# Optimization experiments

Measured on AMD Instinct MI355X. Metric: run time of the kernel, lower is better.

Reference implementation:

```python
import jax, jax.numpy as jnp
import numpy as np

V = 50000      # word vocab
CV = 63        # char vocab (60 chars + 3 tags)
HW = 512       # word hidden size
HC = 256       # char hidden size
NLW = 2        # word lstm layers
NLC = 2        # char lstm layers
L = 12         # chars in the word


def _lstm_layers(x, H, C, Wih, Whh, bih, bhh):
    """One time-step of a multi-layer LSTM (PyTorch gate order i,f,g,o).
    x: [1, D], H/C: [nl, 1, D]. Returns (top_h, newH, newC)."""
    nl = Wih.shape[0]
    newH, newC = [], []
    inp = x
    for l in range(nl):
        gates = inp @ Wih[l].T + H[l] @ Whh[l].T + bih[l] + bhh[l]  # [1, 4D]
        i, f, g, o = jnp.split(gates, 4, axis=-1)
        i = jax.nn.sigmoid(i)
        f = jax.nn.sigmoid(f)
        g = jnp.tanh(g)
        o = jax.nn.sigmoid(o)
        c = f * C[l] + i * g
        h = o * jnp.tanh(c)
        newH.append(h)
        newC.append(c)
        inp = h
    return inp, jnp.stack(newH), jnp.stack(newC)


def setup_inputs() -> dict:
    key = jax.random.key(0)
    ks = jax.random.split(key, 20)
    sW = 1.0 / np.sqrt(HW)
    sC = 1.0 / np.sqrt(HC)
    return {
        "x_word": jax.random.randint(ks[0], (1,), 0, V),
        "x_char": jax.random.randint(ks[1], (L,), 0, CV),
        "h_word_h": jax.random.normal(ks[2], (NLW, 1, HW), jnp.float32),
        "h_word_c": jax.random.normal(ks[3], (NLW, 1, HW), jnp.float32),
        "h_char_h": jax.random.normal(ks[4], (NLC, 1, HC), jnp.float32),
        "h_char_c": jax.random.normal(ks[5], (NLC, 1, HC), jnp.float32),
        "word_emb": jax.random.normal(ks[6], (V, HW), jnp.float32),
        "word_Wih": jax.random.normal(ks[7], (NLW, 4 * HW, HW), jnp.float32) * sW,
        "word_Whh": jax.random.normal(ks[8], (NLW, 4 * HW, HW), jnp.float32) * sW,
        "word_bih": jax.random.normal(ks[9], (NLW, 4 * HW), jnp.float32) * sW,
        "word_bhh": jax.random.normal(ks[10], (NLW, 4 * HW), jnp.float32) * sW,
        "dec_W": jax.random.normal(ks[11], (V, HW), jnp.float32) * sW,
        "dec_b": jax.random.normal(ks[12], (V,), jnp.float32) * sW,
        "char_emb": jax.random.normal(ks[13], (CV, HC), jnp.float32),
        "char_Wih": jax.random.normal(ks[14], (NLC, 4 * HC, HC), jnp.float32) * sC,
        "char_Whh": jax.random.normal(ks[15], (NLC, 4 * HC, HC), jnp.float32) * sC,
        "char_bih": jax.random.normal(ks[16], (NLC, 4 * HC), jnp.float32) * sC,
        "char_bhh": jax.random.normal(ks[17], (NLC, 4 * HC), jnp.float32) * sC,
        "char_to_embedding": jax.random.normal(ks[18], (HW, HC), jnp.float32),
        "g_w": jax.random.normal(ks[19], (HW,), jnp.float32) * sW,
        "g_b": jax.random.normal(jax.random.fold_in(key, 99), (1,), jnp.float32),
    }


def reference(x_word, x_char, h_word_h, h_word_c, h_char_h, h_char_c,
              word_emb, word_Wih, word_Whh, word_bih, word_bhh,
              dec_W, dec_b,
              char_emb, char_Wih, char_Whh, char_bih, char_bhh,
              char_to_embedding, g_w, g_b):
    # character-level recurrence over the word's characters
    def char_step(carry, cidx):
        H, C = carry
        xc = char_emb[cidx][None, :]  # [1, HC]
        _, H, C = _lstm_layers(xc, H, C, char_Wih, char_Whh, char_bih, char_bhh)
        return (H, C), None

    (h_char_h, h_char_c), _ = jax.lax.scan(char_step, (h_char_h, h_char_c), x_char)

    # note: original uses h_char[1] (the CELL state) of the last layer
    x_c = char_to_embedding @ h_char_c[-1].T          # [HW, 1]
    x_w = word_emb[x_word[0]][None, :]                # [1, HW]
    g = jax.nn.relu(jnp.dot(g_w, x_w[0]) + g_b[0])    # scalar gate
    x = (1.0 - g) * x_w + g * x_c.T                   # [1, HW]

    y, h_word_h, h_word_c = _lstm_layers(x, h_word_h, h_word_c,
                                         word_Wih, word_Whh, word_bih, word_bhh)
    y = y @ dec_W.T + dec_b                           # [1, V]
    return y, h_word_h, h_word_c, h_char_h, h_char_c
```

## Files before the change

### kernel.cpp

```cpp
#include <hip/hip_runtime.h>
#include <stdint.h>


static __device__ __forceinline__ float dot4(float4 w, const float* p){
    return w.x*p[0] + w.y*p[1] + w.z*p[2] + w.w*p[3];
}
static __device__ __forceinline__ float sigf(float x){ return 1.0f / (1.0f + __expf(-x)); }
static __device__ __forceinline__ float tanhf_(float x){
    x = fminf(fmaxf(x, -15.0f), 15.0f);
    float e = __expf(2.0f * x);
    return (e - 1.0f) / (e + 1.0f);
}


__global__ __launch_bounds__(256) void k_char(
    int t,
    const int* __restrict__ x_char,
    const float* __restrict__ hch, const float* __restrict__ hcc,
    const float* __restrict__ char_emb,
    const float* __restrict__ cWih, const float* __restrict__ cWhh,
    const float* __restrict__ cbih, const float* __restrict__ cbhh,
    const float* __restrict__ word_emb, const int* __restrict__ x_word,
    const float* __restrict__ g_w, const float* __restrict__ g_b,
    float* __restrict__ ws)
{
    const int tid = threadIdx.x;
    const int bx = blockIdx.x;

    if (bx == 64){
        if (t == 0){
            __shared__ float sw[4];
            const size_t wbase = (size_t)x_word[0] * 512;
            float p = g_w[2*tid]   * word_emb[wbase + 2*tid]
                    + g_w[2*tid+1] * word_emb[wbase + 2*tid+1];
            #pragma unroll
            for (int m = 32; m >= 1; m >>= 1) p += __shfl_xor(p, m, 64);
            if ((tid & 63) == 0) sw[tid >> 6] = p;
            __syncthreads();
            if (tid == 0){
                float gg = sw[0] + sw[1] + sw[2] + sw[3] + g_b[0];
                ws[3072] = fmaxf(gg, 0.0f);
            }
        }
        return;
    }

    __shared__ float sH1[256];
    __shared__ float sH2[256];
    __shared__ float sE[256];
    __shared__ float sg1[16], sg2[16];

    float* h1b = ws;
    float* h2b = ws + 512;
    float* c1  = ws + 1024;
    float* c2  = ws + 1280;

    sH1[tid] = (t == 0) ? hch[tid] : h1b[(t & 1)*256 + tid];
    if (t >= 1) sH2[tid] = (t == 1) ? hch[256 + tid] : h2b[((t-1) & 1)*256 + tid];
    if (t < 12) sE[tid] = char_emb[x_char[t]*256 + tid];
    __syncthreads();

    const int rg = tid >> 4;
    const int lane16 = tid & 15;
    const int gate = rg & 3;
    const int uu = rg >> 2;
    const int u = (bx << 2) + uu;
    const int row = (gate << 8) + u;

    float a1 = 0.f, a2 = 0.f;
    if (t < 12){
        const float4* wi = (const float4*)(cWih + (size_t)row*256) + lane16*4;
        const float4* wh = (const float4*)(cWhh + (size_t)row*256) + lane16*4;
        const float* xp = sE  + lane16*16;
        const float* hp = sH1 + lane16*16;
        #pragma unroll
        for (int j = 0; j < 4; ++j) a1 += dot4(wi[j], xp + 4*j) + dot4(wh[j], hp + 4*j);
    }
    if (t >= 1){
        const size_t r2 = (size_t)(1024 + row);
        const float4* wi = (const float4*)(cWih + r2*256) + lane16*4;
        const float4* wh = (const float4*)(cWhh + r2*256) + lane16*4;
        const float* xp = sH1 + lane16*16;
        const float* hp = sH2 + lane16*16;
        #pragma unroll
        for (int j = 0; j < 4; ++j) a2 += dot4(wi[j], xp + 4*j) + dot4(wh[j], hp + 4*j);
    }
    #pragma unroll
    for (int m = 8; m >= 1; m >>= 1){
        a1 += __shfl_xor(a1, m, 64);
        a2 += __shfl_xor(a2, m, 64);
    }
    if (lane16 == 0){
        if (t < 12) sg1[rg] = a1 + cbih[row]        + cbhh[row];
        if (t >= 1) sg2[rg] = a2 + cbih[1024 + row] + cbhh[1024 + row];
    }
    __syncthreads();

    if (tid < 4){
        if (t < 12){
            int uh = (bx << 2) + tid;
            float gi = sigf(sg1[tid*4+0]);
            float gf = sigf(sg1[tid*4+1]);
            float gg = tanhf_(sg1[tid*4+2]);
            float go = sigf(sg1[tid*4+3]);
            float cp = (t == 0) ? hcc[uh] : c1[uh];
            float c = gf * cp + gi * gg;
            c1[uh] = c;
            h1b[((t+1) & 1)*256 + uh] = go * tanhf_(c);
        }
    } else if (tid < 8){
        if (t >= 1){
            int q = tid - 4;
            int uh = (bx << 2) + q;
            float gi = sigf(sg2[q*4+0]);
            float gf = sigf(sg2[q*4+1]);
            float gg = tanhf_(sg2[q*4+2]);
            float go = sigf(sg2[q*4+3]);
            float cp = (t == 1) ? hcc[256 + uh] : c2[uh];
            float c = gf * cp + gi * gg;
            c2[uh] = c;
            h2b[(t & 1)*256 + uh] = go * tanhf_(c);
        }
    }
}

__global__ __launch_bounds__(256) void k_mix(
    const float* __restrict__ cte, float* __restrict__ ws,
    float* __restrict__ out)
{
    const int tid = threadIdx.x;
    const int bx = blockIdx.x;
    __shared__ float sC2[256];
    sC2[tid] = ws[1280 + tid];
    __syncthreads();

    if (tid < 4){
        int uh = (bx << 2) + tid;
        out[52048 + uh]       = ws[uh];
        out[52048 + 256 + uh] = ws[512 + uh];
        out[52560 + uh]       = ws[1024 + uh];
        out[52560 + 256 + uh] = ws[1280 + uh];
    }
    const int rr = tid >> 5;
    const int lane32 = tid & 31;
    const int row = (bx << 3) + rr;
    const float4* wp = (const float4*)(cte + (size_t)row*256) + lane32*2;
    float acc = dot4(wp[0], sC2 + lane32*8) + dot4(wp[1], sC2 + lane32*8 + 4);
    #pragma unroll
    for (int m = 16; m >= 1; m >>= 1) acc += __shfl_xor(acc, m, 64);
    if (lane32 == 0) ws[1536 + row] = acc;
}

__global__ __launch_bounds__(256) void k_word(
    int l,
    const float* __restrict__ hwh, const float* __restrict__ hwc,
    const float* __restrict__ word_emb, const int* __restrict__ x_word,
    const float* __restrict__ wWih, const float* __restrict__ wWhh,
    const float* __restrict__ wbih, const float* __restrict__ wbhh,
    float* __restrict__ ws, float* __restrict__ out)
{
    const int tid = threadIdx.x;
    const int bx = blockIdx.x;
    __shared__ float sX[512];
    __shared__ float sg[32];

    if (l == 0){
        const size_t wbase = (size_t)x_word[0] * 512;
        float g = ws[3072];
        sX[2*tid]   = (1.0f - g) * word_emb[wbase + 2*tid]   + g * ws[1536 + 2*tid];
        sX[2*tid+1] = (1.0f - g) * word_emb[wbase + 2*tid+1] + g * ws[1536 + 2*tid+1];
    } else {
        sX[2*tid]   = ws[2048 + 2*tid];
        sX[2*tid+1] = ws[2048 + 2*tid+1];
    }
    __syncthreads();

    const int rg8 = tid >> 3;
    const int lane8 = tid & 7;
    const int gate = rg8 & 3;
    const int uu = rg8 >> 2;
    const int uw = (bx << 3) + uu;
    const int row = (gate << 9) + uw;
    const size_t rf = (size_t)(l*2048 + row);

    const float4* wi = (const float4*)(wWih + rf*512) + lane8*16;
    const float4* wh = (const float4*)(wWhh + rf*512) + lane8*16;
    const float4* hv = (const float4*)(hwh + l*512) + lane8*16;
    const float* xp = sX + lane8*64;
    float acc = 0.f;
    #pragma unroll
    for (int j = 0; j < 16; ++j){
        float4 h4 = hv[j];
        acc += dot4(wi[j], xp + 4*j);
        float4 w4 = wh[j];
        acc += w4.x*h4.x + w4.y*h4.y + w4.z*h4.z + w4.w*h4.w;
    }
    #pragma unroll
    for (int m = 4; m >= 1; m >>= 1) acc += __shfl_xor(acc, m, 64);
    if (lane8 == 0) sg[rg8] = acc + wbih[rf] + wbhh[rf];
    __syncthreads();

    if (tid < 8){
        int u2 = (bx << 3) + tid;
        float gi = sigf(sg[tid*4+0]);
        float gf = sigf(sg[tid*4+1]);
        float gg = tanhf_(sg[tid*4+2]);
        float go = sigf(sg[tid*4+3]);
        float c = gf * hwc[l*512 + u2] + gi * gg;
        float h = go * tanhf_(c);
        ws[2048 + l*512 + u2] = h;
        out[50000 + l*512 + u2] = h;
        out[51024 + l*512 + u2] = c;
    }
}

__global__ __launch_bounds__(256) void k_dec(
    const float* __restrict__ dec_W, const float* __restrict__ dec_b,
    const float* __restrict__ h2, float* __restrict__ out)
{
    const int lane = threadIdx.x & 63;
    const int wid = (blockIdx.x * blockDim.x + threadIdx.x) >> 6;
    const int nw = (gridDim.x * blockDim.x) >> 6;
    const float4* hp = (const float4*)h2 + lane*2;
    float4 ha = hp[0], hb = hp[1];
    float hx0[4] = {ha.x, ha.y, ha.z, ha.w};
    float hx1[4] = {hb.x, hb.y, hb.z, hb.w};
    for (int r = wid; r < 50000; r += nw){
        const float4* wp = (const float4*)(dec_W + (size_t)r*512) + lane*2;
        float acc = dot4(wp[0], hx0) + dot4(wp[1], hx1);
        #pragma unroll
        for (int m = 32; m >= 1; m >>= 1) acc += __shfl_xor(acc, m, 64);
        if (lane == 0) out[r] = acc + dec_b[r];
    }
}

extern "C" void kernel_launch(void* const* d_in, const int* in_sizes, int n_in,
                              void* d_out, int out_size, void* d_ws, size_t ws_size,
                              hipStream_t stream)
{
    const int*   x_word   = (const int*)d_in[0];
    const int*   x_char   = (const int*)d_in[1];
    const float* hwh      = (const float*)d_in[2];
    const float* hwc      = (const float*)d_in[3];
    const float* hch      = (const float*)d_in[4];
    const float* hcc      = (const float*)d_in[5];
    const float* word_emb = (const float*)d_in[6];
    const float* wWih     = (const float*)d_in[7];
    const float* wWhh     = (const float*)d_in[8];
    const float* wbih     = (const float*)d_in[9];
    const float* wbhh     = (const float*)d_in[10];
    const float* dec_W    = (const float*)d_in[11];
    const float* dec_b    = (const float*)d_in[12];
    const float* char_emb = (const float*)d_in[13];
    const float* cWih     = (const float*)d_in[14];
    const float* cWhh     = (const float*)d_in[15];
    const float* cbih     = (const float*)d_in[16];
    const float* cbhh     = (const float*)d_in[17];
    const float* cte      = (const float*)d_in[18];
    const float* g_w      = (const float*)d_in[19];
    const float* g_b      = (const float*)d_in[20];

    float* ws = (float*)d_ws;
    float* out = (float*)d_out;

    for (int t = 0; t <= 12; ++t){
        hipLaunchKernelGGL(k_char, dim3(65), dim3(256), 0, stream,
            t, x_char, hch, hcc, char_emb, cWih, cWhh, cbih, cbhh,
            word_emb, x_word, g_w, g_b, ws);
    }
    hipLaunchKernelGGL(k_mix, dim3(64), dim3(256), 0, stream, cte, ws, out);
    hipLaunchKernelGGL(k_word, dim3(64), dim3(256), 0, stream,
        0, hwh, hwc, word_emb, x_word, wWih, wWhh, wbih, wbhh, ws, out);
    hipLaunchKernelGGL(k_word, dim3(64), dim3(256), 0, stream,
        1, hwh, hwc, word_emb, x_word, wWih, wWhh, wbih, wbhh, ws, out);
    hipLaunchKernelGGL(k_dec, dim3(625), dim3(256), 0, stream,
        dec_W, dec_b, ws + 2560, out);
}
```

Before: 332.1 us.

## Fuse all stages into one persistent kernel with atomic grid barriers and decoder prefetch

Replaces the 17 separate launches (13 char steps, mix, two word layers, decoder) with a single 320-block persistent kernel that synchronises stages through agent-scope atomic counters. Char and word LSTM weights are held in registers across timesteps, and idle blocks touch dec_W while waiting so it is already in cache. The point is to remove per-launch overhead and the repeated weight reloads. In exchange it relies on all 320 blocks being co-resident, since otherwise the spin-waits could deadlock, and the polling adds some contention.

```diff
diff --git a/kernel.cpp b/kernel.cpp
--- a/kernel.cpp
+++ b/kernel.cpp
@@ -2,8 +2,13 @@
 #include <stdint.h>
 
 
+#define SCOPE_AGT __HIP_MEMORY_SCOPE_AGENT
+
 static __device__ __forceinline__ float dot4(float4 w, const float* p){
     return w.x*p[0] + w.y*p[1] + w.z*p[2] + w.w*p[3];
+}
+static __device__ __forceinline__ float dot44(float4 a, float4 b){
+    return a.x*b.x + a.y*b.y + a.z*b.z + a.w*b.w;
 }
 static __device__ __forceinline__ float sigf(float x){ return 1.0f / (1.0f + __expf(-x)); }
 static __device__ __forceinline__ float tanhf_(float x){
@@ -11,226 +16,285 @@
     float e = __expf(2.0f * x);
     return (e - 1.0f) / (e + 1.0f);
 }
-
-
-__global__ __launch_bounds__(256) void k_char(
-    int t,
-    const int* __restrict__ x_char,
+static __device__ __forceinline__ void arrive(int* c){
+    __hip_atomic_fetch_add(c, 1, __ATOMIC_RELEASE, SCOPE_AGT);
+}
+static __device__ __forceinline__ void wait_ge(int* c, int tgt){
+    while (__hip_atomic_load(c, __ATOMIC_ACQUIRE, SCOPE_AGT) < tgt)
+        __builtin_amdgcn_s_sleep(2);
+}
+
+static __device__ __forceinline__ void dec_prefetch(const float* __restrict__ dec_W,
+                                                    int* c, int tgt, int wid, int lane){
+    float pf = 0.f;
+    int stop = 0, it = 0;
+    for (int r = wid; r < 50000; r += 1280, ++it){
+        if ((it & 7) == 0){
+            if (lane == 0) stop = (__hip_atomic_load(c, __ATOMIC_RELAXED, SCOPE_AGT) >= tgt);
+            stop = __shfl(stop, 0, 64);
+            if (stop) break;
+        }
+        pf += dec_W[(size_t)r * 512 + lane * 8];
+    }
+    asm volatile("" :: "v"(pf));
+}
+
+__global__ __launch_bounds__(256, 2) void k_fused(
+    const int* __restrict__ x_word, const int* __restrict__ x_char,
+    const float* __restrict__ hwh, const float* __restrict__ hwc,
     const float* __restrict__ hch, const float* __restrict__ hcc,
+    const float* __restrict__ word_emb,
+    const float* __restrict__ wWih, const float* __restrict__ wWhh,
+    const float* __restrict__ wbih, const float* __restrict__ wbhh,
+    const float* __restrict__ dec_W, const float* __restrict__ dec_b,
     const float* __restrict__ char_emb,
     const float* __restrict__ cWih, const float* __restrict__ cWhh,
     const float* __restrict__ cbih, const float* __restrict__ cbhh,
-    const float* __restrict__ word_emb, const int* __restrict__ x_word,
+    const float* __restrict__ cte,
     const float* __restrict__ g_w, const float* __restrict__ g_b,
-    float* __restrict__ ws)
+    float* __restrict__ ws, float* __restrict__ out)
 {
-    const int tid = threadIdx.x;
-    const int bx = blockIdx.x;
-
-    if (bx == 64){
-        if (t == 0){
+    const int tid  = threadIdx.x;
+    const int bx   = blockIdx.x;
+    const int lane = tid & 63;
+    const int wv   = tid >> 6;
+    int* cnt = (int*)(ws + 4096);
+
+    if (bx < 64){
+        __shared__ float sH1[256], sH2[256], sE[256], sg1[16], sg2[16];
+        float* h1b = ws;
+        float* h2b = ws + 512;
+        float* c1  = ws + 1024;
+        float* c2  = ws + 1280;
+
+        const int rg = tid >> 4, lane16 = tid & 15;
+        const int gate = rg & 3, uu = rg >> 2;
+        const int u = (bx << 2) + uu;
+        const int row = (gate << 8) + u, row2 = 1024 + row;
+
+        float4 w1i[4], w1h[4], w2i[4], w2h[4];
+        {
+            const float4* p1i = (const float4*)(cWih + (size_t)row  * 256) + lane16 * 4;
+            const float4* p1h = (const float4*)(cWhh + (size_t)row  * 256) + lane16 * 4;
+            const float4* p2i = (const float4*)(cWih + (size_t)row2 * 256) + lane16 * 4;
+            const float4* p2h = (const float4*)(cWhh + (size_t)row2 * 256) + lane16 * 4;
+            #pragma unroll
+            for (int j = 0; j < 4; ++j){ w1i[j]=p1i[j]; w1h[j]=p1h[j]; w2i[j]=p2i[j]; w2h[j]=p2h[j]; }
+        }
+        const float b1 = cbih[row]  + cbhh[row];
+        const float b2 = cbih[row2] + cbhh[row2];
+
+        for (int t = 0; t <= 12; ++t){
+            sH1[tid] = (t == 0) ? hch[tid] : h1b[(t & 1)*256 + tid];
+            if (t >= 1) sH2[tid] = (t == 1) ? hch[256 + tid] : h2b[((t-1) & 1)*256 + tid];
+            if (t < 12) sE[tid] = char_emb[x_char[t]*256 + tid];
+            __syncthreads();
+
+            float a1 = 0.f, a2 = 0.f;
+            if (t < 12){
+                const float* xp = sE  + lane16*16;
+                const float* hp = sH1 + lane16*16;
+                #pragma unroll
+                for (int j = 0; j < 4; ++j) a1 += dot4(w1i[j], xp + 4*j) + dot4(w1h[j], hp + 4*j);
+            }
+            if (t >= 1){
+                const float* xp = sH1 + lane16*16;
+                const float* hp = sH2 + lane16*16;
+                #pragma unroll
+                for (int j = 0; j < 4; ++j) a2 += dot4(w2i[j], xp + 4*j) + dot4(w2h[j], hp + 4*j);
+            }
+            #pragma unroll
+            for (int m = 8; m >= 1; m >>= 1){
+                a1 += __shfl_xor(a1, m, 64);
+                a2 += __shfl_xor(a2, m, 64);
+            }
+            if (lane16 == 0){
+                if (t < 12) sg1[rg] = a1 + b1;
+                if (t >= 1) sg2[rg] = a2 + b2;
+            }
+            __syncthreads();
+
+            if (tid < 4){
+                if (t < 12){
+                    int uh = (bx << 2) + tid;
+                    float gi = sigf(sg1[tid*4+0]);
+                    float gf = sigf(sg1[tid*4+1]);
+                    float gg = tanhf_(sg1[tid*4+2]);
+                    float go = sigf(sg1[tid*4+3]);
+                    float cp = (t == 0) ? hcc[uh] : c1[uh];
+                    float c = gf * cp + gi * gg;
+                    c1[uh] = c;
+                    h1b[((t+1) & 1)*256 + uh] = go * tanhf_(c);
+                }
+            } else if (tid < 8){
+                if (t >= 1){
+                    int q = tid - 4;
+                    int uh = (bx << 2) + q;
+                    float gi = sigf(sg2[q*4+0]);
+                    float gf = sigf(sg2[q*4+1]);
+                    float gg = tanhf_(sg2[q*4+2]);
+                    float go = sigf(sg2[q*4+3]);
+                    float cp = (t == 1) ? hcc[256 + uh] : c2[uh];
+                    float c = gf * cp + gi * gg;
+                    c2[uh] = c;
+                    h2b[(t & 1)*256 + uh] = go * tanhf_(c);
+                }
+            }
+            __syncthreads();
+            if (tid == 0){
+                arrive(&cnt[0]);
+                if (t < 12) wait_ge(&cnt[0], 64*(t+1));
+            }
+            __syncthreads();
+        }
+        if (tid < 4){
+            int uh = (bx << 2) + tid;
+            out[52048 + uh]       = h1b[uh];
+            out[52048 + 256 + uh] = h2b[uh];
+            out[52560 + uh]       = c1[uh];
+            out[52560 + 256 + uh] = c2[uh];
+        }
+        dec_prefetch(dec_W, &cnt[3], 128, (bx << 2) + wv, lane);
+
+    } else if (bx < 192){
+        const int vw = ((bx - 64) << 2) + wv;
+        float4 wi0[4], wi1[4], wh0[4], wh1[4]; float bs[4];
+        #pragma unroll
+        for (int gq = 0; gq < 4; ++gq){
+            const size_t rf = (size_t)((gq << 9) + vw);
+            const float4* pi = (const float4*)(wWih + rf*512) + lane*2;
+            const float4* ph = (const float4*)(wWhh + rf*512) + lane*2;
+            wi0[gq] = pi[0]; wi1[gq] = pi[1];
+            wh0[gq] = ph[0]; wh1[gq] = ph[1];
+            bs[gq] = wbih[rf] + wbhh[rf];
+        }
+        const float4* hv = (const float4*)(hwh) + lane*2;
+        const float4 hva = hv[0], hvb = hv[1];
+        const size_t wbase = (size_t)x_word[0] * 512;
+        const float4* wep = (const float4*)(word_emb + wbase) + lane*2;
+        const float4 wea = wep[0], web = wep[1];
+
+        if (bx == 64){
             __shared__ float sw[4];
-            const size_t wbase = (size_t)x_word[0] * 512;
             float p = g_w[2*tid]   * word_emb[wbase + 2*tid]
                     + g_w[2*tid+1] * word_emb[wbase + 2*tid+1];
             #pragma unroll
             for (int m = 32; m >= 1; m >>= 1) p += __shfl_xor(p, m, 64);
-            if ((tid & 63) == 0) sw[tid >> 6] = p;
-            __syncthreads();
-            if (tid == 0){
-                float gg = sw[0] + sw[1] + sw[2] + sw[3] + g_b[0];
-                ws[3072] = fmaxf(gg, 0.0f);
-            }
-        }
-        return;
+            if (lane == 0) sw[wv] = p;
+            __syncthreads();
+            if (tid == 0) ws[3072] = fmaxf(sw[0]+sw[1]+sw[2]+sw[3] + g_b[0], 0.0f);
+        }
+
+        if (tid == 0) wait_ge(&cnt[0], 64*13);
+        __syncthreads();
+
+        {
+            float4 cv  = ((const float4*)(cte + (size_t)vw*256))[lane];
+            float4 c2v = ((const float4*)(ws + 1280))[lane];
+            float acc = dot44(cv, c2v);
+            #pragma unroll
+            for (int m = 32; m >= 1; m >>= 1) acc += __shfl_xor(acc, m, 64);
+            if (lane == 0) ws[1536 + vw] = acc;
+        }
+        __syncthreads();
+        if (tid == 0){ arrive(&cnt[1]); wait_ge(&cnt[1], 128); }
+        __syncthreads();
+
+        {
+            const float g  = ws[3072];
+            const float og = 1.0f - g;
+            const float4* xc = (const float4*)(ws + 1536) + lane*2;
+            const float4 x0 = xc[0], x1 = xc[1];
+            float4 xa, xb;
+            xa.x = og*wea.x + g*x0.x; xa.y = og*wea.y + g*x0.y;
+            xa.z = og*wea.z + g*x0.z; xa.w = og*wea.w + g*x0.w;
+            xb.x = og*web.x + g*x1.x; xb.y = og*web.y + g*x1.y;
+            xb.z = og*web.z + g*x1.z; xb.w = og*web.w + g*x1.w;
+            float ac[4];
+            #pragma unroll
+            for (int gq = 0; gq < 4; ++gq){
+                float a = dot44(wi0[gq], xa) + dot44(wi1[gq], xb)
+                        + dot44(wh0[gq], hva) + dot44(wh1[gq], hvb);
+                #pragma unroll
+                for (int m = 32; m >= 1; m >>= 1) a += __shfl_xor(a, m, 64);
+                ac[gq] = a;
+            }
+            if (lane == 0){
+                float gi = sigf(ac[0] + bs[0]);
+                float gf = sigf(ac[1] + bs[1]);
+                float gg = tanhf_(ac[2] + bs[2]);
+                float go = sigf(ac[3] + bs[3]);
+                float c = gf * hwc[vw] + gi * gg;
+                float h = go * tanhf_(c);
+                ws[2048 + vw]  = h;
+                out[50000 + vw] = h;
+                out[51024 + vw] = c;
+            }
+        }
+        __syncthreads();
+        if (tid == 0) arrive(&cnt[2]);
+        dec_prefetch(dec_W, &cnt[3], 128, (bx << 2) + wv, lane);
+
+    } else {
+        const int vw = ((bx - 192) << 2) + wv;
+        float4 wi0[4], wi1[4], wh0[4], wh1[4]; float bs[4];
+        #pragma unroll
+        for (int gq = 0; gq < 4; ++gq){
+            const size_t rf = (size_t)(2048 + (gq << 9) + vw);
+            const float4* pi = (const float4*)(wWih + rf*512) + lane*2;
+            const float4* ph = (const float4*)(wWhh + rf*512) + lane*2;
+            wi0[gq] = pi[0]; wi1[gq] = pi[1];
+            wh0[gq] = ph[0]; wh1[gq] = ph[1];
+            bs[gq] = wbih[rf] + wbhh[rf];
+        }
+        const float4* hv = (const float4*)(hwh + 512) + lane*2;
+        const float4 hva = hv[0], hvb = hv[1];
+
+        dec_prefetch(dec_W, &cnt[2], 128, (bx << 2) + wv, lane);
+
+        if (tid == 0) wait_ge(&cnt[2], 128);
+        __syncthreads();
+        {
+            const float4* xc = (const float4*)(ws + 2048) + lane*2;
+            const float4 xa = xc[0], xb = xc[1];
+            float ac[4];
+            #pragma unroll
+            for (int gq = 0; gq < 4; ++gq){
+                float a = dot44(wi0[gq], xa) + dot44(wi1[gq], xb)
+                        + dot44(wh0[gq], hva) + dot44(wh1[gq], hvb);
+                #pragma unroll
+                for (int m = 32; m >= 1; m >>= 1) a += __shfl_xor(a, m, 64);
+                ac[gq] = a;
+            }
+            if (lane == 0){
+                float gi = sigf(ac[0] + bs[0]);
+                float gf = sigf(ac[1] + bs[1]);
+                float gg = tanhf_(ac[2] + bs[2]);
+                float go = sigf(ac[3] + bs[3]);
+                float c = gf * hwc[512 + vw] + gi * gg;
+                float h = go * tanhf_(c);
+                ws[2560 + vw]        = h;
+                out[50000 + 512 + vw] = h;
+                out[51024 + 512 + vw] = c;
+            }
+        }
+        __syncthreads();
+        if (tid == 0) arrive(&cnt[3]);
     }
 
-    __shared__ float sH1[256];
-    __shared__ float sH2[256];
-    __shared__ float sE[256];
-    __shared__ float sg1[16], sg2[16];
-
-    float* h1b = ws;
-    float* h2b = ws + 512;
-    float* c1  = ws + 1024;
-    float* c2  = ws + 1280;
-
-    sH1[tid] = (t == 0) ? hch[tid] : h1b[(t & 1)*256 + tid];
-    if (t >= 1) sH2[tid] = (t == 1) ? hch[256 + tid] : h2b[((t-1) & 1)*256 + tid];
-    if (t < 12) sE[tid] = char_emb[x_char[t]*256 + tid];
+    if (tid == 0) wait_ge(&cnt[3], 128);
     __syncthreads();
-
-    const int rg = tid >> 4;
-    const int lane16 = tid & 15;
-    const int gate = rg & 3;
-    const int uu = rg >> 2;
-    const int u = (bx << 2) + uu;
-    const int row = (gate << 8) + u;
-
-    float a1 = 0.f, a2 = 0.f;
-    if (t < 12){
-        const float4* wi = (const float4*)(cWih + (size_t)row*256) + lane16*4;
-        const float4* wh = (const float4*)(cWhh + (size_t)row*256) + lane16*4;
-        const float* xp = sE  + lane16*16;
-        const float* hp = sH1 + lane16*16;
-        #pragma unroll
-        for (int j = 0; j < 4; ++j) a1 += dot4(wi[j], xp + 4*j) + dot4(wh[j], hp + 4*j);
-    }
-    if (t >= 1){
-        const size_t r2 = (size_t)(1024 + row);
-        const float4* wi = (const float4*)(cWih + r2*256) + lane16*4;
-        const float4* wh = (const float4*)(cWhh + r2*256) + lane16*4;
-        const float* xp = sH1 + lane16*16;
-        const float* hp = sH2 + lane16*16;
-        #pragma unroll
-        for (int j = 0; j < 4; ++j) a2 += dot4(wi[j], xp + 4*j) + dot4(wh[j], hp + 4*j);
-    }
-    #pragma unroll
-    for (int m = 8; m >= 1; m >>= 1){
-        a1 += __shfl_xor(a1, m, 64);
-        a2 += __shfl_xor(a2, m, 64);
-    }
-    if (lane16 == 0){
-        if (t < 12) sg1[rg] = a1 + cbih[row]        + cbhh[row];
-        if (t >= 1) sg2[rg] = a2 + cbih[1024 + row] + cbhh[1024 + row];
-    }
-    __syncthreads();
-
-    if (tid < 4){
-        if (t < 12){
-            int uh = (bx << 2) + tid;
-            float gi = sigf(sg1[tid*4+0]);
-            float gf = sigf(sg1[tid*4+1]);
-            float gg = tanhf_(sg1[tid*4+2]);
-            float go = sigf(sg1[tid*4+3]);
-            float cp = (t == 0) ? hcc[uh] : c1[uh];
-            float c = gf * cp + gi * gg;
-            c1[uh] = c;
-            h1b[((t+1) & 1)*256 + uh] = go * tanhf_(c);
-        }
-    } else if (tid < 8){
-        if (t >= 1){
-            int q = tid - 4;
-            int uh = (bx << 2) + q;
-            float gi = sigf(sg2[q*4+0]);
-            float gf = sigf(sg2[q*4+1]);
-            float gg = tanhf_(sg2[q*4+2]);
-            float go = sigf(sg2[q*4+3]);
-            float cp = (t == 1) ? hcc[256 + uh] : c2[uh];
-            float c = gf * cp + gi * gg;
-            c2[uh] = c;
-            h2b[(t & 1)*256 + uh] = go * tanhf_(c);
-        }
-    }
-}
-
-__global__ __launch_bounds__(256) void k_mix(
-    const float* __restrict__ cte, float* __restrict__ ws,
-    float* __restrict__ out)
-{
-    const int tid = threadIdx.x;
-    const int bx = blockIdx.x;
-    __shared__ float sC2[256];
-    sC2[tid] = ws[1280 + tid];
-    __syncthreads();
-
-    if (tid < 4){
-        int uh = (bx << 2) + tid;
-        out[52048 + uh]       = ws[uh];
-        out[52048 + 256 + uh] = ws[512 + uh];
-        out[52560 + uh]       = ws[1024 + uh];
-        out[52560 + 256 + uh] = ws[1280 + uh];
-    }
-    const int rr = tid >> 5;
-    const int lane32 = tid & 31;
-    const int row = (bx << 3) + rr;
-    const float4* wp = (const float4*)(cte + (size_t)row*256) + lane32*2;
-    float acc = dot4(wp[0], sC2 + lane32*8) + dot4(wp[1], sC2 + lane32*8 + 4);
-    #pragma unroll
-    for (int m = 16; m >= 1; m >>= 1) acc += __shfl_xor(acc, m, 64);
-    if (lane32 == 0) ws[1536 + row] = acc;
-}
-
-__global__ __launch_bounds__(256) void k_word(
-    int l,
-    const float* __restrict__ hwh, const float* __restrict__ hwc,
-    const float* __restrict__ word_emb, const int* __restrict__ x_word,
-    const float* __restrict__ wWih, const float* __restrict__ wWhh,
-    const float* __restrict__ wbih, const float* __restrict__ wbhh,
-    float* __restrict__ ws, float* __restrict__ out)
-{
-    const int tid = threadIdx.x;
-    const int bx = blockIdx.x;
-    __shared__ float sX[512];
-    __shared__ float sg[32];
-
-    if (l == 0){
-        const size_t wbase = (size_t)x_word[0] * 512;
-        float g = ws[3072];
-        sX[2*tid]   = (1.0f - g) * word_emb[wbase + 2*tid]   + g * ws[1536 + 2*tid];
-        sX[2*tid+1] = (1.0f - g) * word_emb[wbase + 2*tid+1] + g * ws[1536 + 2*tid+1];
-    } else {
-        sX[2*tid]   = ws[2048 + 2*tid];
-        sX[2*tid+1] = ws[2048 + 2*tid+1];
-    }
-    __syncthreads();
-
-    const int rg8 = tid >> 3;
-    const int lane8 = tid & 7;
-    const int gate = rg8 & 3;
-    const int uu = rg8 >> 2;
-    const int uw = (bx << 3) + uu;
-    const int row = (gate << 9) + uw;
-    const size_t rf = (size_t)(l*2048 + row);
-
-    const float4* wi = (const float4*)(wWih + rf*512) + lane8*16;
-    const float4* wh = (const float4*)(wWhh + rf*512) + lane8*16;
-    const float4* hv = (const float4*)(hwh + l*512) + lane8*16;
-    const float* xp = sX + lane8*64;
-    float acc = 0.f;
-    #pragma unroll
-    for (int j = 0; j < 16; ++j){
-        float4 h4 = hv[j];
-        acc += dot4(wi[j], xp + 4*j);
-        float4 w4 = wh[j];
-        acc += w4.x*h4.x + w4.y*h4.y + w4.z*h4.z + w4.w*h4.w;
-    }
-    #pragma unroll
-    for (int m = 4; m >= 1; m >>= 1) acc += __shfl_xor(acc, m, 64);
-    if (lane8 == 0) sg[rg8] = acc + wbih[rf] + wbhh[rf];
-    __syncthreads();
-
-    if (tid < 8){
-        int u2 = (bx << 3) + tid;
-        float gi = sigf(sg[tid*4+0]);
-        float gf = sigf(sg[tid*4+1]);
-        float gg = tanhf_(sg[tid*4+2]);
-        float go = sigf(sg[tid*4+3]);
-        float c = gf * hwc[l*512 + u2] + gi * gg;
-        float h = go * tanhf_(c);
-        ws[2048 + l*512 + u2] = h;
-        out[50000 + l*512 + u2] = h;
-        out[51024 + l*512 + u2] = c;
-    }
-}
-
-__global__ __launch_bounds__(256) void k_dec(
-    const float* __restrict__ dec_W, const float* __restrict__ dec_b,
-    const float* __restrict__ h2, float* __restrict__ out)
-{
-    const int lane = threadIdx.x & 63;
-    const int wid = (blockIdx.x * blockDim.x + threadIdx.x) >> 6;
-    const int nw = (gridDim.x * blockDim.x) >> 6;
-    const float4* hp = (const float4*)h2 + lane*2;
-    float4 ha = hp[0], hb = hp[1];
-    float hx0[4] = {ha.x, ha.y, ha.z, ha.w};
-    float hx1[4] = {hb.x, hb.y, hb.z, hb.w};
-    for (int r = wid; r < 50000; r += nw){
-        const float4* wp = (const float4*)(dec_W + (size_t)r*512) + lane*2;
-        float acc = dot4(wp[0], hx0) + dot4(wp[1], hx1);
-        #pragma unroll
-        for (int m = 32; m >= 1; m >>= 1) acc += __shfl_xor(acc, m, 64);
-        if (lane == 0) out[r] = acc + dec_b[r];
+    {
+        const float4* hp = (const float4*)(ws + 2560) + lane*2;
+        const float4 ha = hp[0], hb = hp[1];
+        const int wid = (bx << 2) + wv;
+        for (int r = wid; r < 50000; r += 1280){
+            const float4* wp = (const float4*)(dec_W + (size_t)r*512) + lane*2;
+            float acc = dot44(wp[0], ha) + dot44(wp[1], hb);
+            #pragma unroll
+            for (int m = 32; m >= 1; m >>= 1) acc += __shfl_xor(acc, m, 64);
+            if (lane == 0) out[r] = acc + dec_b[r];
+        }
     }
 }
 
@@ -260,19 +324,14 @@
     const float* g_w      = (const float*)d_in[19];
     const float* g_b      = (const float*)d_in[20];
 
-    float* ws = (float*)d_ws;
+    float* ws  = (float*)d_ws;
     float* out = (float*)d_out;
 
-    for (int t = 0; t <= 12; ++t){
-        hipLaunchKernelGGL(k_char, dim3(65), dim3(256), 0, stream,
-            t, x_char, hch, hcc, char_emb, cWih, cWhh, cbih, cbhh,
-            word_emb, x_word, g_w, g_b, ws);
-    }
-    hipLaunchKernelGGL(k_mix, dim3(64), dim3(256), 0, stream, cte, ws, out);
-    hipLaunchKernelGGL(k_word, dim3(64), dim3(256), 0, stream,
-        0, hwh, hwc, word_emb, x_word, wWih, wWhh, wbih, wbhh, ws, out);
-    hipLaunchKernelGGL(k_word, dim3(64), dim3(256), 0, stream,
-        1, hwh, hwc, word_emb, x_word, wWih, wWhh, wbih, wbhh, ws, out);
-    hipLaunchKernelGGL(k_dec, dim3(625), dim3(256), 0, stream,
-        dec_W, dec_b, ws + 2560, out);
-}
+    hipMemsetAsync((void*)((char*)d_ws + 16384), 0, 64, stream);
+
+    hipLaunchKernelGGL(k_fused, dim3(320), dim3(256), 0, stream,
+        x_word, x_char, hwh, hwc, hch, hcc, word_emb,
+        wWih, wWhh, wbih, wbhh, dec_W, dec_b,
+        char_emb, cWih, cWhh, cbih, cbhh, cte, g_w, g_b,
+        ws, out);
+}
```

Result: slower. 594.9 us (+79.1%).
